# Optimization experiments

Hardware: AMD Instinct MI355X
Metric: run time of the kernel (lower is better)

## Reference

```python
import jax, jax.numpy as jnp
import numpy as np

NUM_HEADS = 16
HEAD_DIM = 64


def setup_inputs() -> dict:
    key = jax.random.key(0)
    ks = jax.random.split(key, 9)
    B, S, E = 16, 577, 1024
    return {
        "hidden_states": jax.random.normal(ks[0], (B, S, E), dtype=jnp.float32),
        "q_w": jax.random.normal(ks[1], (E, E), dtype=jnp.float32) * 0.02,
        "q_b": jax.random.normal(ks[2], (E,), dtype=jnp.float32) * 0.02,
        "v_w": jax.random.normal(ks[3], (E, E), dtype=jnp.float32) * 0.02,
        "v_b": jax.random.normal(ks[4], (E,), dtype=jnp.float32) * 0.02,
        "out_w": jax.random.normal(ks[5], (E, E), dtype=jnp.float32) * 0.02,
        "out_b": jax.random.normal(ks[6], (E,), dtype=jnp.float32) * 0.02,
        "share_key": jax.random.normal(ks[7], (1, NUM_HEADS, HEAD_DIM, 1), dtype=jnp.float32) * 0.1,
        "share_bias": jax.random.normal(ks[8], (NUM_HEADS, S, S), dtype=jnp.float32) * 0.05,
        "layer": 10,
    }


def reference(hidden_states, q_w, q_b, v_w, v_b, out_w, out_b, share_key, share_bias, layer):
    # layer >= START_SHARE_LAYER (9): ShareKey.cal_attention branch.
    B, S, E = hidden_states.shape
    H, D = NUM_HEADS, HEAD_DIM
    scale = D ** -0.5

    # projections (torch Linear: x @ W.T + b)
    q = (hidden_states @ q_w.T + q_b) * scale          # [B,S,E]
    v = hidden_states @ v_w.T + v_b                    # [B,S,E]
    q = q.reshape(B, S, H, D).transpose(0, 2, 1, 3)    # [B,H,S,D]
    v = v.reshape(B, S, H, D).transpose(0, 2, 1, 3)    # [B,H,S,D]

    # rank-1 learned-key scores: matmul(q, key[1,H,D,1]) -> [B,H,S,1]
    scores = jnp.einsum("bhsd,hd->bhs", q, share_key[0, :, :, 0])  # [B,H,S]
    # expand along last axis to [B,H,S,S] and add per-layer learned bias
    attn = scores[..., None] + share_bias[None]         # [B,H,S,S]
    attn = jax.nn.softmax(attn, axis=-1)

    # attn @ V, merge heads, output projection
    out = jnp.einsum("bhij,bhjd->bhid", attn, v)        # [B,H,S,D]
    out = out.transpose(0, 2, 1, 3).reshape(B, S, E)
    out = out @ out_w.T + out_b
    return out
```

## Files before the change

kernel.cpp:

```cpp
#include <hip/hip_runtime.h>


typedef __attribute__((ext_vector_type(4))) float f32x4;
typedef __attribute__((ext_vector_type(4))) unsigned int u32x4;

__device__ __forceinline__ unsigned short f2h(float f) {
  union { _Float16 h; unsigned short u; } x;
  x.h = (_Float16)f;
  return x.u;
}

__device__ __forceinline__ void mfma16(f32x4& d, u32x4 a, u32x4 b) {
  asm("v_mfma_f32_16x16x32_f16 %0, %1, %2, %0" : "+v"(d) : "v"(a), "v"(b));
}

__device__ __forceinline__ void gl_lds16(const unsigned short* g, unsigned short* l) {
  __builtin_amdgcn_global_load_lds(
      (const __attribute__((address_space(1))) unsigned int*)g,
      (__attribute__((address_space(3))) unsigned int*)l, 16, 0, 0);
}

__global__ __launch_bounds__(256) void prep_hs_kernel(const float* __restrict__ X,
                                                      unsigned short* __restrict__ Y) {
  int idx = blockIdx.x * 256 + threadIdx.x;
  int n = idx << 2;
  int row = n >> 10;
  int col = n & 1023;
  int b = row / 584;
  int s = row - b * 584;
  unsigned short o0 = 0, o1 = 0, o2 = 0, o3 = 0;
  if (s < 577) {
    const float4 v = *(const float4*)(X + (((size_t)(b * 577 + s)) << 10) + col);
    o0 = f2h(v.x); o1 = f2h(v.y); o2 = f2h(v.z); o3 = f2h(v.w);
  }
  ushort4 o; o.x = o0; o.y = o1; o.z = o2; o.w = o3;
  *(ushort4*)(Y + n) = o;
}

__global__ __launch_bounds__(256) void prep_w_kernel(const float* __restrict__ X,
                                                     unsigned short* __restrict__ Y) {
  int idx = blockIdx.x * 256 + threadIdx.x;
  int n = idx << 2;
  const float4 v = *(const float4*)(X + n);
  ushort4 o; o.x = f2h(v.x); o.y = f2h(v.y); o.z = f2h(v.z); o.w = f2h(v.w);
  *(ushort4*)(Y + n) = o;
}

__global__ __launch_bounds__(256) void softmax_kernel(const float* __restrict__ SB,
                                                      unsigned short* __restrict__ P) {
  const int i = blockIdx.x;
  const int h = blockIdx.y;
  unsigned short* prow = P + ((size_t)h * 640 + i) * 608;
  const int tid = threadIdx.x;
  if (i >= 577) {
    for (int j = tid; j < 608; j += 256) prow[j] = 0;
    return;
  }
  const float* row = SB + ((size_t)h * 577 + i) * 577;
  __shared__ float buf[577];
  __shared__ float redm[4];
  __shared__ float reds[4];
  float lmax = -3.0e38f;
  for (int j = tid; j < 577; j += 256) { float v = row[j]; buf[j] = v; lmax = fmaxf(lmax, v); }
  #pragma unroll
  for (int off = 32; off > 0; off >>= 1) lmax = fmaxf(lmax, __shfl_xor(lmax, off));
  if ((tid & 63) == 0) redm[tid >> 6] = lmax;
  __syncthreads();
  const float m = fmaxf(fmaxf(redm[0], redm[1]), fmaxf(redm[2], redm[3]));
  float lsum = 0.f;
  for (int j = tid; j < 577; j += 256) { float e = __expf(buf[j] - m); buf[j] = e; lsum += e; }
  #pragma unroll
  for (int off = 32; off > 0; off >>= 1) lsum += __shfl_xor(lsum, off);
  if ((tid & 63) == 0) reds[tid >> 6] = lsum;
  __syncthreads();
  const float inv = 1.f / (reds[0] + reds[1] + reds[2] + reds[3]);
  for (int j = tid; j < 608; j += 256)
    prow[j] = (j < 577) ? f2h(buf[j] * inv) : (unsigned short)0;
}

template<int MODE>
__global__ __launch_bounds__(256) void gemm_db_kernel(
    const unsigned short* __restrict__ A, int lda,
    const unsigned short* __restrict__ B, int ldb,
    const float* __restrict__ bias,
    void* __restrict__ Cv, int ldc, int K)
{
  __shared__ unsigned short As0[128 * 32];
  __shared__ unsigned short Bs0[128 * 32];
  __shared__ unsigned short As1[128 * 32];
  __shared__ unsigned short Bs1[128 * 32];
  const int tid  = threadIdx.x;
  const int lane = tid & 63;
  const int w    = tid >> 6;
  const int wm = w >> 1, wn = w & 1;
  const int l15 = lane & 15, lhi = lane >> 4;
  const int lr = lane >> 2, lc = (lane & 3) << 3;

  const int nwg8 = (int)gridDim.x >> 3;
  const int orig = blockIdx.x;
  const int id = (orig & 7) * nwg8 + (orig >> 3);
  int mt, nt, hh = 0;
  if (MODE == 1)      { hh = id / 40; const int r = id - hh * 40; nt = r & 7; mt = r >> 3; }
  else if (MODE == 0) { mt = id & 7;  nt = id >> 3; }
  else                { nt = id & 7;  mt = id >> 3; }
  const int m0 = mt * 128, n0 = nt * 128;

  const unsigned short* Abase = (MODE == 1) ? A + (size_t)hh * 640 * 608 : A;
  const unsigned short* gA0 = Abase + (size_t)(m0 + w * 32 + lr) * lda + lc;
  const unsigned short* gA1 = gA0 + (size_t)16 * lda;
  const unsigned short* gB0;
  const unsigned short* gB1;
  if (MODE == 1) {
    const int nb0 = n0 + w * 32 + lr;
    const int nb1 = nb0 + 16;
    gB0 = B + (size_t)(hh * 64 + (nb0 & 63)) * 9344 + (nb0 >> 6) * 584 + lc;
    gB1 = B + (size_t)(hh * 64 + (nb1 & 63)) * 9344 + (nb1 >> 6) * 584 + lc;
  } else {
    gB0 = B + (size_t)(n0 + w * 32 + lr) * ldb + lc;
    gB1 = gB0 + (size_t)16 * ldb;
  }

  f32x4 acc[4][4] = {};
  const int NT = K >> 5;

#define STAGE(AS, BS, k0)                         \
  do {                                            \
    gl_lds16(gA0 + (k0), (AS) + w * 1024);        \
    gl_lds16(gA1 + (k0), (AS) + w * 1024 + 512);  \
    gl_lds16(gB0 + (k0), (BS) + w * 1024);        \
    gl_lds16(gB1 + (k0), (BS) + w * 1024 + 512);  \
  } while (0)

#define COMPUTE(AS, BS)                                                        \
  do {                                                                         \
    u32x4 af[4], bv[4];                                                        \
    _Pragma("unroll")                                                          \
    for (int i = 0; i < 4; i++)                                                \
      af[i] = *(const u32x4*)&(AS)[(wm * 64 + i * 16 + l15) * 32 + (lhi << 3)];\
    _Pragma("unroll")                                                          \
    for (int i = 0; i < 4; i++)                                                \
      bv[i] = *(const u32x4*)&(BS)[(wn * 64 + i * 16 + l15) * 32 + (lhi << 3)];\
    _Pragma("unroll")                                                          \
    for (int i = 0; i < 4; i++)                                                \
      _Pragma("unroll")                                                        \
      for (int j = 0; j < 4; j++)                                              \
        mfma16(acc[i][j], af[i], bv[j]);                                       \
  } while (0)

  STAGE(As0, Bs0, 0);
  __syncthreads();
  for (int kt = 0; kt < NT; kt += 2) {
    if (kt + 1 < NT) STAGE(As1, Bs1, (kt + 1) << 5);
    COMPUTE(As0, Bs0);
    __syncthreads();
    if (kt + 1 < NT) {
      if (kt + 2 < NT) STAGE(As0, Bs0, (kt + 2) << 5);
      COMPUTE(As1, Bs1);
      __syncthreads();
    }
  }
#undef STAGE
#undef COMPUTE

  const int rb = m0 + wm * 64 + (lhi << 2);
  const int cb = n0 + wn * 64 + l15;
  #pragma unroll
  for (int i = 0; i < 4; i++) {
    #pragma unroll
    for (int r = 0; r < 4; r++) {
      const int row = rb + i * 16 + r;
      if (MODE == 0) {
        const float rbias = bias[row];
        #pragma unroll
        for (int j = 0; j < 4; j++) {
          const int col = cb + j * 16;
          ((unsigned short*)Cv)[(size_t)row * ldc + col] = f2h(acc[i][j][r] + rbias);
        }
      } else if (MODE == 1) {
        if (row < 577) {
          #pragma unroll
          for (int j = 0; j < 4; j++) {
            const int n = cb + j * 16;
            const int b = n >> 6, d = n & 63;
            ((unsigned short*)Cv)[(((size_t)b * 577 + row) << 10) + hh * 64 + d] =
                f2h(acc[i][j][r]);
          }
        }
      } else {
        if (row < 9232) {
          #pragma unroll
          for (int j = 0; j < 4; j++) {
            const int col = cb + j * 16;
            ((float*)Cv)[(size_t)row * ldc + col] = acc[i][j][r] + bias[col];
          }
        }
      }
    }
  }
}

extern "C" void kernel_launch(void* const* d_in, const int* in_sizes, int n_in,
                              void* d_out, int out_size, void* d_ws, size_t ws_size,
                              hipStream_t stream) {
  (void)in_sizes; (void)n_in; (void)out_size; (void)ws_size;
  const float* hs    = (const float*)d_in[0];
  const float* v_w   = (const float*)d_in[3];
  const float* v_b   = (const float*)d_in[4];
  const float* out_w = (const float*)d_in[5];
  const float* out_b = (const float*)d_in[6];
  const float* sb    = (const float*)d_in[8];
  float* out = (float*)d_out;

  char* ws = (char*)d_ws;
  constexpr size_t HS_SZ = (size_t)9344 * 1024 * 2;
  constexpr size_t W_SZ  = (size_t)1024 * 1024 * 2;
  constexpr size_t VT_SZ = (size_t)1024 * 9344 * 2 + 256;
  unsigned short* hs_f16 = (unsigned short*)(ws);
  unsigned short* vw_f16 = (unsigned short*)(ws + HS_SZ);
  unsigned short* ow_f16 = (unsigned short*)(ws + HS_SZ + W_SZ);
  unsigned short* vt     = (unsigned short*)(ws + HS_SZ + 2 * W_SZ);
  unsigned short* pmat   = (unsigned short*)(ws + HS_SZ + 2 * W_SZ + VT_SZ);

  prep_hs_kernel<<<9344, 256, 0, stream>>>(hs, hs_f16);
  prep_w_kernel<<<1024, 256, 0, stream>>>(v_w, vw_f16);
  prep_w_kernel<<<1024, 256, 0, stream>>>(out_w, ow_f16);
  softmax_kernel<<<dim3(640, 16), 256, 0, stream>>>(sb, pmat);
  gemm_db_kernel<0><<<584, 256, 0, stream>>>(vw_f16, 1024, hs_f16, 1024, v_b,
                                             (void*)vt, 9344, 1024);
  gemm_db_kernel<1><<<640, 256, 0, stream>>>(pmat, 608, vt, 0, nullptr,
                                             (void*)hs_f16, 0, 608);
  gemm_db_kernel<2><<<584, 256, 0, stream>>>(hs_f16, 1024, ow_f16, 1024, out_b,
                                             (void*)out, 1024, 1024);
}
```

Before: 213.6 us.

## Merge prep kernels into one launch and shrink GEMM tiles to 64x128

Four preprocessing launches (hidden-state cast, two weight casts, softmax of the bias) become one kernel that dispatches on block index, which removes launch overhead and gaps between launches. The three GEMMs move from 128x128 to 64x128 output tiles with a new k-major LDS layout and 4x2 MFMA fragments per wave. This doubles the block count so the 256 CUs get better occupancy and load balance. The cost is less operand reuse per tile and more global and LDS traffic per FLOP.

```diff
diff --git a/kernel.cpp b/kernel.cpp
--- a/kernel.cpp
+++ b/kernel.cpp
@@ -20,46 +20,50 @@
       (__attribute__((address_space(3))) unsigned int*)l, 16, 0, 0);
 }
 
-__global__ __launch_bounds__(256) void prep_hs_kernel(const float* __restrict__ X,
-                                                      unsigned short* __restrict__ Y) {
-  int idx = blockIdx.x * 256 + threadIdx.x;
-  int n = idx << 2;
-  int row = n >> 10;
-  int col = n & 1023;
-  int b = row / 584;
-  int s = row - b * 584;
-  unsigned short o0 = 0, o1 = 0, o2 = 0, o3 = 0;
-  if (s < 577) {
-    const float4 v = *(const float4*)(X + (((size_t)(b * 577 + s)) << 10) + col);
-    o0 = f2h(v.x); o1 = f2h(v.y); o2 = f2h(v.z); o3 = f2h(v.w);
-  }
-  ushort4 o; o.x = o0; o.y = o1; o.z = o2; o.w = o3;
-  *(ushort4*)(Y + n) = o;
-}
-
-__global__ __launch_bounds__(256) void prep_w_kernel(const float* __restrict__ X,
-                                                     unsigned short* __restrict__ Y) {
-  int idx = blockIdx.x * 256 + threadIdx.x;
-  int n = idx << 2;
-  const float4 v = *(const float4*)(X + n);
-  ushort4 o; o.x = f2h(v.x); o.y = f2h(v.y); o.z = f2h(v.z); o.w = f2h(v.w);
-  *(ushort4*)(Y + n) = o;
-}
-
-__global__ __launch_bounds__(256) void softmax_kernel(const float* __restrict__ SB,
-                                                      unsigned short* __restrict__ P) {
-  const int i = blockIdx.x;
-  const int h = blockIdx.y;
+__global__ __launch_bounds__(256) void prep_all_kernel(
+    const float* __restrict__ HS, const float* __restrict__ VW,
+    const float* __restrict__ OW, const float* __restrict__ SB,
+    unsigned short* __restrict__ hsY, unsigned short* __restrict__ vwY,
+    unsigned short* __restrict__ owY, unsigned short* __restrict__ P)
+{
+  __shared__ float buf[577];
+  __shared__ float redm[4];
+  __shared__ float reds[4];
+  const int bid = blockIdx.x;
+  const int tid = threadIdx.x;
+
+  if (bid < 9344) {
+    const int row = bid;
+    const int b = row / 584;
+    const int s = row - b * 584;
+    const int col = tid << 2;
+    ushort4 o = {0, 0, 0, 0};
+    if (s < 577) {
+      const float4 v = *(const float4*)(HS + (((size_t)(b * 577 + s)) << 10) + col);
+      o.x = f2h(v.x); o.y = f2h(v.y); o.z = f2h(v.z); o.w = f2h(v.w);
+    }
+    *(ushort4*)(hsY + ((size_t)row << 10) + col) = o;
+    return;
+  }
+  if (bid < 11392) {
+    const int r = bid - 9344;
+    const float* X = (r < 1024) ? VW : OW;
+    unsigned short* Y = (r < 1024) ? vwY : owY;
+    const int n = ((r & 1023) << 10) + (tid << 2);
+    const float4 v = *(const float4*)(X + n);
+    ushort4 o; o.x = f2h(v.x); o.y = f2h(v.y); o.z = f2h(v.z); o.w = f2h(v.w);
+    *(ushort4*)(Y + n) = o;
+    return;
+  }
+  const int r = bid - 11392;
+  const int h = r / 640;
+  const int i = r - h * 640;
   unsigned short* prow = P + ((size_t)h * 640 + i) * 608;
-  const int tid = threadIdx.x;
   if (i >= 577) {
     for (int j = tid; j < 608; j += 256) prow[j] = 0;
     return;
   }
   const float* row = SB + ((size_t)h * 577 + i) * 577;
-  __shared__ float buf[577];
-  __shared__ float redm[4];
-  __shared__ float reds[4];
   float lmax = -3.0e38f;
   for (int j = tid; j < 577; j += 256) { float v = row[j]; buf[j] = v; lmax = fmaxf(lmax, v); }
   #pragma unroll
@@ -79,72 +83,67 @@
 }
 
 template<int MODE>
-__global__ __launch_bounds__(256) void gemm_db_kernel(
+__global__ __launch_bounds__(256) void gemm64_kernel(
     const unsigned short* __restrict__ A, int lda,
     const unsigned short* __restrict__ B, int ldb,
     const float* __restrict__ bias,
     void* __restrict__ Cv, int ldc, int K)
 {
-  __shared__ unsigned short As0[128 * 32];
+  __shared__ unsigned short As0[64 * 32];
   __shared__ unsigned short Bs0[128 * 32];
-  __shared__ unsigned short As1[128 * 32];
+  __shared__ unsigned short As1[64 * 32];
   __shared__ unsigned short Bs1[128 * 32];
   const int tid  = threadIdx.x;
   const int lane = tid & 63;
   const int w    = tid >> 6;
-  const int wm = w >> 1, wn = w & 1;
   const int l15 = lane & 15, lhi = lane >> 4;
-  const int lr = lane >> 2, lc = (lane & 3) << 3;
 
   const int nwg8 = (int)gridDim.x >> 3;
   const int orig = blockIdx.x;
   const int id = (orig & 7) * nwg8 + (orig >> 3);
   int mt, nt, hh = 0;
-  if (MODE == 1)      { hh = id / 40; const int r = id - hh * 40; nt = r & 7; mt = r >> 3; }
-  else if (MODE == 0) { mt = id & 7;  nt = id >> 3; }
+  if (MODE == 1)      { hh = id / 80; const int r = id - hh * 80; mt = r % 10; nt = r / 10; }
+  else if (MODE == 0) { mt = id & 15; nt = id >> 4; }
   else                { nt = id & 7;  mt = id >> 3; }
-  const int m0 = mt * 128, n0 = nt * 128;
+  const int m0 = mt * 64, n0 = nt * 128;
 
   const unsigned short* Abase = (MODE == 1) ? A + (size_t)hh * 640 * 608 : A;
-  const unsigned short* gA0 = Abase + (size_t)(m0 + w * 32 + lr) * lda + lc;
-  const unsigned short* gA1 = gA0 + (size_t)16 * lda;
+  const unsigned short* gA = Abase + (size_t)(m0 + lane) * lda + w * 8;
   const unsigned short* gB0;
   const unsigned short* gB1;
   if (MODE == 1) {
-    const int nb0 = n0 + w * 32 + lr;
-    const int nb1 = nb0 + 16;
-    gB0 = B + (size_t)(hh * 64 + (nb0 & 63)) * 9344 + (nb0 >> 6) * 584 + lc;
-    gB1 = B + (size_t)(hh * 64 + (nb1 & 63)) * 9344 + (nb1 >> 6) * 584 + lc;
+    const int nb0 = n0 + lane, nb1 = n0 + 64 + lane;
+    gB0 = B + (size_t)(hh * 64 + (nb0 & 63)) * 9344 + (nb0 >> 6) * 584 + w * 8;
+    gB1 = B + (size_t)(hh * 64 + (nb1 & 63)) * 9344 + (nb1 >> 6) * 584 + w * 8;
   } else {
-    gB0 = B + (size_t)(n0 + w * 32 + lr) * ldb + lc;
-    gB1 = gB0 + (size_t)16 * ldb;
-  }
-
-  f32x4 acc[4][4] = {};
+    gB0 = B + (size_t)(n0 + lane) * ldb + w * 8;
+    gB1 = gB0 + (size_t)64 * ldb;
+  }
+
+  f32x4 acc[4][2] = {};
   const int NT = K >> 5;
 
-#define STAGE(AS, BS, k0)                         \
-  do {                                            \
-    gl_lds16(gA0 + (k0), (AS) + w * 1024);        \
-    gl_lds16(gA1 + (k0), (AS) + w * 1024 + 512);  \
-    gl_lds16(gB0 + (k0), (BS) + w * 1024);        \
-    gl_lds16(gB1 + (k0), (BS) + w * 1024 + 512);  \
+#define STAGE(AS, BS, k0)                       \
+  do {                                          \
+    gl_lds16(gA + (k0), (AS) + w * 512);        \
+    gl_lds16(gB0 + (k0), (BS) + w * 1024);      \
+    gl_lds16(gB1 + (k0), (BS) + w * 1024 + 512);\
   } while (0)
 
-#define COMPUTE(AS, BS)                                                        \
-  do {                                                                         \
-    u32x4 af[4], bv[4];                                                        \
-    _Pragma("unroll")                                                          \
-    for (int i = 0; i < 4; i++)                                                \
-      af[i] = *(const u32x4*)&(AS)[(wm * 64 + i * 16 + l15) * 32 + (lhi << 3)];\
-    _Pragma("unroll")                                                          \
-    for (int i = 0; i < 4; i++)                                                \
-      bv[i] = *(const u32x4*)&(BS)[(wn * 64 + i * 16 + l15) * 32 + (lhi << 3)];\
-    _Pragma("unroll")                                                          \
-    for (int i = 0; i < 4; i++)                                                \
-      _Pragma("unroll")                                                        \
-      for (int j = 0; j < 4; j++)                                              \
-        mfma16(acc[i][j], af[i], bv[j]);                                       \
+#define COMPUTE(AS, BS)                                                  \
+  do {                                                                   \
+    u32x4 af[4], bv[2];                                                  \
+    _Pragma("unroll")                                                    \
+    for (int i = 0; i < 4; i++)                                          \
+      af[i] = *(const u32x4*)&(AS)[(lhi * 64 + i * 16 + l15) * 8];       \
+    _Pragma("unroll")                                                    \
+    for (int j = 0; j < 2; j++)                                          \
+      bv[j] = *(const u32x4*)&(BS)[(lhi * 128 + w * 32 + j * 16 + l15) * 8];\
+    _Pragma("unroll")                                                    \
+    for (int i = 0; i < 4; i++)                                          \
+      _Pragma("unroll")                                                  \
+      for (int j = 0; j < 2; j++)                                        \
+        mfma16(acc[i][j], af[i], bv[j]);                                 \
   } while (0)
 
   STAGE(As0, Bs0, 0);
@@ -162,25 +161,23 @@
 #undef STAGE
 #undef COMPUTE
 
-  const int rb = m0 + wm * 64 + (lhi << 2);
-  const int cb = n0 + wn * 64 + l15;
   #pragma unroll
   for (int i = 0; i < 4; i++) {
     #pragma unroll
     for (int r = 0; r < 4; r++) {
-      const int row = rb + i * 16 + r;
+      const int row = m0 + i * 16 + (lhi << 2) + r;
       if (MODE == 0) {
         const float rbias = bias[row];
         #pragma unroll
-        for (int j = 0; j < 4; j++) {
-          const int col = cb + j * 16;
+        for (int j = 0; j < 2; j++) {
+          const int col = n0 + w * 32 + j * 16 + l15;
           ((unsigned short*)Cv)[(size_t)row * ldc + col] = f2h(acc[i][j][r] + rbias);
         }
       } else if (MODE == 1) {
         if (row < 577) {
           #pragma unroll
-          for (int j = 0; j < 4; j++) {
-            const int n = cb + j * 16;
+          for (int j = 0; j < 2; j++) {
+            const int n = n0 + w * 32 + j * 16 + l15;
             const int b = n >> 6, d = n & 63;
             ((unsigned short*)Cv)[(((size_t)b * 577 + row) << 10) + hh * 64 + d] =
                 f2h(acc[i][j][r]);
@@ -189,8 +186,8 @@
       } else {
         if (row < 9232) {
           #pragma unroll
-          for (int j = 0; j < 4; j++) {
-            const int col = cb + j * 16;
+          for (int j = 0; j < 2; j++) {
+            const int col = n0 + w * 32 + j * 16 + l15;
             ((float*)Cv)[(size_t)row * ldc + col] = acc[i][j][r] + bias[col];
           }
         }
@@ -221,14 +218,12 @@
   unsigned short* vt     = (unsigned short*)(ws + HS_SZ + 2 * W_SZ);
   unsigned short* pmat   = (unsigned short*)(ws + HS_SZ + 2 * W_SZ + VT_SZ);
 
-  prep_hs_kernel<<<9344, 256, 0, stream>>>(hs, hs_f16);
-  prep_w_kernel<<<1024, 256, 0, stream>>>(v_w, vw_f16);
-  prep_w_kernel<<<1024, 256, 0, stream>>>(out_w, ow_f16);
-  softmax_kernel<<<dim3(640, 16), 256, 0, stream>>>(sb, pmat);
-  gemm_db_kernel<0><<<584, 256, 0, stream>>>(vw_f16, 1024, hs_f16, 1024, v_b,
+  prep_all_kernel<<<21632, 256, 0, stream>>>(hs, v_w, out_w, sb,
+                                             hs_f16, vw_f16, ow_f16, pmat);
+  gemm64_kernel<0><<<1168, 256, 0, stream>>>(vw_f16, 1024, hs_f16, 1024, v_b,
                                              (void*)vt, 9344, 1024);
-  gemm_db_kernel<1><<<640, 256, 0, stream>>>(pmat, 608, vt, 0, nullptr,
+  gemm64_kernel<1><<<1280, 256, 0, stream>>>(pmat, 608, vt, 0, nullptr,
                                              (void*)hs_f16, 0, 608);
-  gemm_db_kernel<2><<<584, 256, 0, stream>>>(hs_f16, 1024, ow_f16, 1024, out_b,
+  gemm64_kernel<2><<<1168, 256, 0, stream>>>(hs_f16, 1024, ow_f16, 1024, out_b,
                                              (void*)out, 1024, 1024);
 }
```

Result: slower. 294.1 us (+37.6%).
